# Performance work log

Hardware: AMD Instinct MI355X
Metric: run time of the kernel (lower is better)

Reference implementation:

```python
import jax, jax.numpy as jnp
import numpy as np

B, T, D = 2, 1024, 1024
H, DK = 16, 64  # n_head, d_k; inner dim = H*DK = D
INV_SQRT_DK = 1.0 / float(np.sqrt(DK))


def setup_inputs() -> dict:
    key = jax.random.key(0)
    ks = jax.random.split(key, 16)
    init = lambda k, shape: (jax.random.normal(k, shape, dtype=jnp.float32) * 0.02)
    return {
        "query": jax.random.normal(ks[0], (B, T, D), dtype=jnp.float32),
        "key": jax.random.normal(ks[1], (B, T, D), dtype=jnp.float32),
        "value": jax.random.normal(ks[2], (B, T, D), dtype=jnp.float32),
        "pos_k": jax.random.normal(ks[3], (T, T, DK), dtype=jnp.float32),
        "pos_v": jax.random.normal(ks[4], (T, T, DK), dtype=jnp.float32),
        "mask": jnp.ones((B, T, T), dtype=jnp.int32),
        "relative_attention_bias": jax.random.normal(ks[5], (1, H, T, T), dtype=jnp.float32),
        "Wq": init(ks[6], (D, D)), "bq": init(ks[7], (D,)),
        "Wk": init(ks[8], (D, D)), "bk": init(ks[9], (D,)),
        "Wv": init(ks[10], (D, D)), "bv": init(ks[11], (D,)),
        "Wo": init(ks[12], (D, D)), "bo": init(ks[13], (D,)),
    }


def reference(query, key, value, pos_k, pos_v, mask, relative_attention_bias,
              Wq, bq, Wk, bk, Wv, bv, Wo, bo):
    nb = query.shape[0]
    # projections -> (B, H, T, DK); q pre-scaled by 1/sqrt(d_k)
    q = (query @ Wq + bq).reshape(nb, -1, H, DK).transpose(0, 2, 1, 3) * INV_SQRT_DK
    k = (key @ Wk + bk).reshape(nb, -1, H, DK).transpose(0, 2, 1, 3)
    v = (value @ Wv + bv).reshape(nb, -1, H, DK).transpose(0, 2, 1, 3)

    # content scores + relative-position key scores (B, H, T, S)
    A = jnp.einsum('bhtd,bhsd->bhts', q, k)
    Bp = jnp.einsum('bhtd,tsd->bhts', q, pos_k)
    scores = A + Bp + relative_attention_bias

    # masked softmax: mask (B, T, S) -> invalid where mask == 0
    inv = (mask[:, None, :, :] == 0)  # (B, 1, T, S)
    scores = jnp.where(inv, -jnp.inf, scores)
    attn = jax.nn.softmax(scores, axis=-1)
    attn = jnp.where(inv, 0.0, attn)

    # value aggregation + relative-position value term
    x = jnp.einsum('bhts,bhsd->bhtd', attn, v)
    x = x + jnp.einsum('bhts,tsd->bhtd', attn, pos_v)

    x = x.transpose(0, 2, 1, 3).reshape(nb, -1, H * DK)  # (B, T, D)
    return x @ Wo + bo
```

## Files before the change

### kernel.cpp

```cpp
#include <hip/hip_runtime.h>


#define DEV __device__ __forceinline__

typedef short bf16x8 __attribute__((ext_vector_type(8)));
typedef short bf16x4 __attribute__((ext_vector_type(4)));
typedef float f32x4 __attribute__((ext_vector_type(4)));

DEV short f2b(float f) {
  unsigned u = __builtin_bit_cast(unsigned, f);
  u = (u + 0x7FFFu + ((u >> 16) & 1u)) >> 16;
  return (short)u;
}
DEV float b2f(short s) {
  unsigned u = ((unsigned)(unsigned short)s) << 16;
  return __builtin_bit_cast(float, u);
}

#define MFMA(a, b, c) __builtin_amdgcn_mfma_f32_16x16x32_bf16(a, b, c, 0, 0, 0)

DEV void gload16(const void* g, void* l) {
  __builtin_amdgcn_global_load_lds(
      (const __attribute__((address_space(1))) void*)g,
      (__attribute__((address_space(3))) void*)l, 16, 0, 0);
}

__global__ __launch_bounds__(256) void k_cvt3(
    const float* __restrict__ a, const float* __restrict__ b, const float* __restrict__ c,
    short* __restrict__ oa, short* __restrict__ ob, short* __restrict__ oc) {
  const float* src = blockIdx.y == 0 ? a : (blockIdx.y == 1 ? b : c);
  short* dst = blockIdx.y == 0 ? oa : (blockIdx.y == 1 ? ob : oc);
  size_t i = ((size_t)blockIdx.x * 256 + threadIdx.x) * 8;
  float4 p0 = *(const float4*)(src + i);
  float4 p1 = *(const float4*)(src + i + 4);
  bf16x8 o;
  o[0] = f2b(p0.x); o[1] = f2b(p0.y); o[2] = f2b(p0.z); o[3] = f2b(p0.w);
  o[4] = f2b(p1.x); o[5] = f2b(p1.y); o[6] = f2b(p1.z); o[7] = f2b(p1.w);
  *(bf16x8*)(dst + i) = o;
}

__global__ __launch_bounds__(256) void k_wtrans4(
    const float* __restrict__ w0, const float* __restrict__ w1,
    const float* __restrict__ w2, const float* __restrict__ w3,
    short* __restrict__ o0, short* __restrict__ o1,
    short* __restrict__ o2, short* __restrict__ o3) {
  const float* src; short* dst;
  switch (blockIdx.z) {
    case 0: src = w0; dst = o0; break;
    case 1: src = w1; dst = o1; break;
    case 2: src = w2; dst = o2; break;
    default: src = w3; dst = o3;
  }
  __shared__ short LW[64][74];
  const int tid = threadIdx.x;
  const int k0 = blockIdx.y * 64, n0 = blockIdx.x * 64;
  {
    int c4 = (tid & 15) * 4;
#pragma unroll
    for (int i = 0; i < 4; ++i) {
      int r = (tid >> 4) + i * 16;
      float4 v = *(const float4*)(src + (size_t)(k0 + r) * 1024 + n0 + c4);
      LW[r][c4 + 0] = f2b(v.x); LW[r][c4 + 1] = f2b(v.y);
      LW[r][c4 + 2] = f2b(v.z); LW[r][c4 + 3] = f2b(v.w);
    }
  }
  __syncthreads();
  {
    int n = tid >> 2, kb = (tid & 3) * 16;
#pragma unroll
    for (int j2 = 0; j2 < 2; ++j2) {
      int kk = kb + j2 * 8;
      bf16x8 o;
#pragma unroll
      for (int j = 0; j < 8; ++j) o[j] = LW[kk + j][n];
      *(bf16x8*)(dst + (size_t)(n0 + n) * 1024 + k0 + kk) = o;
    }
  }
}

__global__ __launch_bounds__(256) void k_qkv(
    const short* __restrict__ Ain, const short* __restrict__ WT,
    const float* __restrict__ bq, const float* __restrict__ bk,
    const float* __restrict__ bv,
    short* __restrict__ qo, short* __restrict__ ko, short* __restrict__ vTo) {
  __shared__ short As[128 * 32];
  __shared__ short Bs[64 * 32];
  __shared__ short LW[128][72];
  const int tid = threadIdx.x;
  const int w = tid >> 6, l = tid & 63, lg = l >> 4, lr = l & 15;
  const int wm = w >> 1, wn = w & 1;
  const int flat = blockIdx.x + gridDim.x * blockIdx.y;
  const int flat2 = (flat & 7) * 96 + (flat >> 3);
  const int n0 = (flat2 & 15) * 64;
  const int m0 = (flat2 >> 4) * 128;
  const int seg = m0 >> 11;
  const int mseg = m0 & 2047;
  const short* Abase = Ain + ((size_t)m0 << 10);
  const short* Bbase = WT + ((size_t)seg << 20) + ((size_t)n0 << 10);
  const int srow = l >> 2, scol8 = (l & 3) * 8;
  f32x4 acc[4][2] = {};
  for (int k0 = 0; k0 < 1024; k0 += 32) {
    gload16(Abase + (size_t)((w * 2) * 16 + srow) * 1024 + k0 + scol8, &As[(w * 2) * 512]);
    gload16(Abase + (size_t)((w * 2 + 1) * 16 + srow) * 1024 + k0 + scol8, &As[(w * 2 + 1) * 512]);
    gload16(Bbase + (size_t)(w * 16 + srow) * 1024 + k0 + scol8, &Bs[w * 512]);
    __syncthreads();
    bf16x8 af[4], bf[2];
#pragma unroll
    for (int i = 0; i < 4; ++i) af[i] = *(const bf16x8*)&As[(wm * 64 + i * 16 + lr) * 32 + lg * 8];
#pragma unroll
    for (int i = 0; i < 2; ++i) bf[i] = *(const bf16x8*)&Bs[(wn * 32 + i * 16 + lr) * 32 + lg * 8];
#pragma unroll
    for (int mi = 0; mi < 4; ++mi)
#pragma unroll
      for (int ni = 0; ni < 2; ++ni) acc[mi][ni] = MFMA(af[mi], bf[ni], acc[mi][ni]);
    __syncthreads();
  }
  const float* bias = seg == 0 ? bq : (seg == 1 ? bk : bv);
  const float scale = seg == 0 ? 0.125f : 1.0f;
  float bvals[2];
#pragma unroll
  for (int ni = 0; ni < 2; ++ni) bvals[ni] = bias[n0 + wn * 32 + ni * 16 + lr];
#pragma unroll
  for (int mi = 0; mi < 4; ++mi)
#pragma unroll
    for (int ni = 0; ni < 2; ++ni)
#pragma unroll
      for (int r = 0; r < 4; ++r)
        LW[wm * 64 + mi * 16 + lg * 4 + r][wn * 32 + ni * 16 + lr] =
            f2b((acc[mi][ni][r] + bvals[ni]) * scale);
  __syncthreads();
  if (seg < 2) {
    short* dst = seg == 0 ? qo : ko;
    int r = tid >> 1, half = tid & 1;
    int m = mseg + r, b = m >> 10, t = m & 1023;
    int h = n0 >> 6;
#pragma unroll
    for (int g = 0; g < 4; ++g) {
      int dk = half * 32 + g * 8;
      bf16x8 o = *(const bf16x8*)&LW[r][dk];
      *(bf16x8*)(dst + (((size_t)(b * 16 + h) * 1024 + t) << 6) + dk) = o;
    }
  } else {
    int dkc = tid & 63, th = tid >> 6;
    int h = n0 >> 6, dk = dkc;
    int b = mseg >> 10;
    int tbase = (mseg & 1023) + th * 32;
#pragma unroll
    for (int g = 0; g < 4; ++g) {
      bf16x8 o;
#pragma unroll
      for (int e = 0; e < 8; ++e) o[e] = LW[th * 32 + g * 8 + e][dkc];
      *(bf16x8*)(vTo + (((size_t)(b * 16 + h) * 64 + dk) << 10) + tbase + g * 8) = o;
    }
  }
}

__global__ __launch_bounds__(512, 2) void k_qk(
    const short* __restrict__ q, const short* __restrict__ kmat,
    short* __restrict__ S) {
  const int bh = blockIdx.y;
  const int tid = threadIdx.x;
  const int w = tid >> 6, l = tid & 63, lg = l >> 4, lr = l & 15;
  const int wm = w >> 2, wn = w & 3;
  const int t0 = blockIdx.x * 32 + wm * 16;
  const int scol = wn * 256;
  __shared__ short LS[8][16][266];

  bf16x8 af[2];
#pragma unroll
  for (int kk = 0; kk < 2; ++kk)
    af[kk] = *(const bf16x8*)(q + ((size_t)bh * 1024 + (t0 + lr)) * 64 + kk * 32 + lg * 8);

#pragma unroll
  for (int ni = 0; ni < 16; ++ni) {
    int s = scol + ni * 16 + lr;
    const short* kp = kmat + ((size_t)bh * 1024 + s) * 64 + lg * 8;
    f32x4 a = {};
    a = MFMA(af[0], *(const bf16x8*)kp, a);
    a = MFMA(af[1], *(const bf16x8*)(kp + 32), a);
#pragma unroll
    for (int r = 0; r < 4; ++r) LS[w][lg * 4 + r][ni * 16 + lr] = f2b(a[r]);
  }
  short* sb = S + ((size_t)bh * 1024 + t0) * 1024 + scol;
  const int r2 = l >> 5, c16 = (l & 31) * 8;
#pragma unroll
  for (int rr = 0; rr < 8; ++rr) {
    int row = rr * 2 + r2;
    bf16x8 o = *(const bf16x8*)&LS[w][row][c16];
    *(bf16x8*)(sb + (size_t)row * 1024 + c16) = o;
  }
}

__global__ __launch_bounds__(256) void k_posk_exp(
    const short* __restrict__ q, const float* __restrict__ pos_k,
    const float* __restrict__ rab, const int* __restrict__ mask,
    short* __restrict__ S) {
  const int t = blockIdx.y;
  const int tid = threadIdx.x;
  const int w = tid >> 6, l = tid & 63, lg = l >> 4, lr = l & 15;
  const int sB = blockIdx.x * 256;
  const int s0 = sB + w * 64;
  __shared__ float RB[16][260];
  __shared__ int MK[2][260];
  __shared__ short SW[4][32][66];
  {
    int hr = tid >> 4, c0 = (tid & 15) * 4;
#pragma unroll
    for (int it = 0; it < 4; ++it) {
      int c = c0 + it * 64;
      float4 v = *(const float4*)(rab + ((size_t)hr * 1024 + t) * 1024 + sB + c);
      RB[hr][c] = v.x; RB[hr][c + 1] = v.y; RB[hr][c + 2] = v.z; RB[hr][c + 3] = v.w;
    }
  }
  if (tid < 128) {
    int br = tid >> 6, c = (tid & 63) * 4;
    int4 mv = *(const int4*)(mask + ((size_t)br * 1024 + t) * 1024 + sB + c);
    MK[br][c] = mv.x; MK[br][c + 1] = mv.y; MK[br][c + 2] = mv.z; MK[br][c + 3] = mv.w;
  }
  {
#pragma unroll
    for (int rr = 0; rr < 4; ++rr) {
      int row = (l >> 3) + rr * 8;
      int s8 = (l & 7) * 8;
      *(bf16x8*)&SW[w][row][s8] =
          *(const bf16x8*)(S + ((size_t)row * 1024 + t) * 1024 + s0 + s8);
    }
  }
  bf16x8 af[2][2];
#pragma unroll
  for (int mi = 0; mi < 2; ++mi)
#pragma unroll
    for (int kk = 0; kk < 2; ++kk) {
      int bh = mi * 16 + lr;
      af[mi][kk] = *(const bf16x8*)(q + ((size_t)bh * 1024 + t) * 64 + kk * 32 + lg * 8);
    }
  f32x4 acc[2][4] = {};
#pragma unroll
  for (int ni = 0; ni < 4; ++ni) {
    int s = s0 + ni * 16 + lr;
#pragma unroll
    for (int kk = 0; kk < 2; ++kk) {
      const float* pk = pos_k + ((size_t)t * 1024 + s) * 64 + kk * 32 + lg * 8;
      const float4 p0 = *(const float4*)pk;
      const float4 p1 = *(const float4*)(pk + 4);
      bf16x8 bfr;
      bfr[0] = f2b(p0.x); bfr[1] = f2b(p0.y); bfr[2] = f2b(p0.z); bfr[3] = f2b(p0.w);
      bfr[4] = f2b(p1.x); bfr[5] = f2b(p1.y); bfr[6] = f2b(p1.z); bfr[7] = f2b(p1.w);
#pragma unroll
      for (int mi = 0; mi < 2; ++mi) acc[mi][ni] = MFMA(af[mi][kk], bfr, acc[mi][ni]);
    }
  }
  __syncthreads();
#pragma unroll
  for (int ni = 0; ni < 4; ++ni) {
    int colw = w * 64 + ni * 16 + lr;
    int col = ni * 16 + lr;
    int msk0 = MK[0][colw];
    int msk1 = MK[1][colw];
#pragma unroll
    for (int r = 0; r < 4; ++r) {
      int h = lg * 4 + r;
      float bv = RB[h][colw];
      float v0 = acc[0][ni][r] + bv + b2f(SW[w][h][col]);
      float v1 = acc[1][ni][r] + bv + b2f(SW[w][16 + h][col]);
      float e0 = (msk0 == 0) ? 0.f : __expf(v0 - 10.f);
      float e1 = (msk1 == 0) ? 0.f : __expf(v1 - 10.f);
      SW[w][h][col] = f2b(e0);
      SW[w][16 + h][col] = f2b(e1);
    }
  }
#pragma unroll
  for (int rr = 0; rr < 4; ++rr) {
    int row = (l >> 3) + rr * 8;
    int s8 = (l & 7) * 8;
    bf16x8 o = *(const bf16x8*)&SW[w][row][s8];
    *(bf16x8*)(S + ((size_t)row * 1024 + t) * 1024 + s0 + s8) = o;
  }
}

__global__ __launch_bounds__(256) void k_posv(
    const short* __restrict__ S, const float* __restrict__ pos_v,
    short* __restrict__ X0p) {
  const int half = blockIdx.x;
  const int t = blockIdx.y;
  const int tid = threadIdx.x;
  const int w = tid >> 6, l = tid & 63, lg = l >> 4, lr = l & 15;
  const int mi = w >> 1;
  const int nb = (w & 1) * 2;
  __shared__ short pvT[64][132];
  f32x4 acc[2] = {};
  const int spair = tid >> 4;
  const int dk4 = (tid & 15) * 4;
  const int sbase = half * 512;
  for (int c = 0; c < 4; ++c) {
    const int sc = sbase + c * 128;
    if (c) __syncthreads();
#pragma unroll
    for (int it = 0; it < 4; ++it) {
      int srel = spair * 2 + it * 32;
      const float* p0 = pos_v + ((size_t)t * 1024 + sc + srel) * 64 + dk4;
      float4 a = *(const float4*)p0;
      float4 b = *(const float4*)(p0 + 64);
      unsigned u0 = (unsigned)(unsigned short)f2b(a.x) | ((unsigned)(unsigned short)f2b(b.x) << 16);
      unsigned u1 = (unsigned)(unsigned short)f2b(a.y) | ((unsigned)(unsigned short)f2b(b.y) << 16);
      unsigned u2 = (unsigned)(unsigned short)f2b(a.z) | ((unsigned)(unsigned short)f2b(b.z) << 16);
      unsigned u3 = (unsigned)(unsigned short)f2b(a.w) | ((unsigned)(unsigned short)f2b(b.w) << 16);
      *(unsigned*)&pvT[dk4 + 0][srel] = u0;
      *(unsigned*)&pvT[dk4 + 1][srel] = u1;
      *(unsigned*)&pvT[dk4 + 2][srel] = u2;
      *(unsigned*)&pvT[dk4 + 3][srel] = u3;
    }
    __syncthreads();
    const int bh = mi * 16 + lr;
    const short* sBp = S + ((size_t)bh * 1024 + t) * 1024 + sc;
#pragma unroll
    for (int kk = 0; kk < 4; ++kk) {
      bf16x8 afr = *(const bf16x8*)(sBp + kk * 32 + lg * 8);
#pragma unroll
      for (int ni = 0; ni < 2; ++ni) {
        int dk = (nb + ni) * 16 + lr;
        const short* pp = &pvT[dk][kk * 32 + lg * 8];
        bf16x4 lo = *(const bf16x4*)pp;
        bf16x4 hi = *(const bf16x4*)(pp + 4);
        bf16x8 bfr;
        bfr[0] = lo[0]; bfr[1] = lo[1]; bfr[2] = lo[2]; bfr[3] = lo[3];
        bfr[4] = hi[0]; bfr[5] = hi[1]; bfr[6] = hi[2]; bfr[7] = hi[3];
        acc[ni] = MFMA(afr, bfr, acc[ni]);
      }
    }
  }
#pragma unroll
  for (int ni = 0; ni < 2; ++ni)
#pragma unroll
    for (int r = 0; r < 4; ++r) {
      int bh2 = mi * 16 + lg * 4 + r;
      int b = bh2 >> 4, h = bh2 & 15;
      int dk = (nb + ni) * 16 + lr;
      X0p[((size_t)half << 21) + ((size_t)(b * 1024 + t)) * 1024 + h * 64 + dk] =
          f2b(acc[ni][r]);
    }
}

__global__ __launch_bounds__(256) void k_av(
    const short* __restrict__ S, const short* __restrict__ vT,
    const short* __restrict__ X0p, short* __restrict__ X) {
  const int bh = blockIdx.y;
  const int tt0 = blockIdx.x * 32;
  const int tid = threadIdx.x;
  const int w = tid >> 6, l = tid & 63, lg = l >> 4, lr = l & 15;
  const int wm = w >> 1, wn = w & 1;
  const short* vbase = vT + ((size_t)bh << 16) + ((size_t)(wn * 32) << 10);
  const short* sbase = S + ((size_t)bh << 20) + ((size_t)(tt0 + wm * 16) << 10);
  f32x4 acc[2] = {};
  float lsum = 0.f;
#pragma unroll 8
  for (int kk = 0; kk < 32; ++kk) {
    bf16x8 afr = *(const bf16x8*)(sbase + ((size_t)lr << 10) + kk * 32 + lg * 8);
#pragma unroll
    for (int j = 0; j < 8; ++j) lsum += b2f(afr[j]);
#pragma unroll
    for (int ni = 0; ni < 2; ++ni) {
      bf16x8 bfr = *(const bf16x8*)(vbase + ((size_t)(ni * 16 + lr) << 10) + kk * 32 + lg * 8);
      acc[ni] = MFMA(afr, bfr, acc[ni]);
    }
  }
  lsum += __shfl_xor(lsum, 16);
  lsum += __shfl_xor(lsum, 32);
  const int b = bh >> 4, h = bh & 15;
#pragma unroll
  for (int ni = 0; ni < 2; ++ni)
#pragma unroll
    for (int r = 0; r < 4; ++r) {
      float lrow = __shfl(lsum, lg * 4 + r);
      float inv = 1.0f / lrow;
      int tt = tt0 + wm * 16 + lg * 4 + r;
      int d = h * 64 + wn * 32 + ni * 16 + lr;
      size_t idx = ((size_t)(b * 1024 + tt)) * 1024 + d;
      X[idx] = f2b((b2f(X0p[idx]) + b2f(X0p[idx + (1u << 21)]) + acc[ni][r]) * inv);
    }
}

__global__ __launch_bounds__(256) void k_oproj(
    const short* __restrict__ X, const short* __restrict__ WT,
    const float* __restrict__ bias, float* __restrict__ out) {
  __shared__ short As[64 * 32];
  __shared__ short Bs[64 * 32];
  const int tid = threadIdx.x;
  const int w = tid >> 6, l = tid & 63, lg = l >> 4, lr = l & 15;
  const int wm = w >> 1, wn = w & 1;
  const int n0 = blockIdx.x * 64;
  const int m0 = blockIdx.y * 64;
  const short* Abase = X + ((size_t)m0 << 10);
  const short* Bbase = WT + ((size_t)n0 << 10);
  const int srow = l >> 2, scol8 = (l & 3) * 8;
  f32x4 acc[2][2] = {};
  for (int k0 = 0; k0 < 1024; k0 += 32) {
    gload16(Abase + (size_t)(w * 16 + srow) * 1024 + k0 + scol8, &As[w * 512]);
    gload16(Bbase + (size_t)(w * 16 + srow) * 1024 + k0 + scol8, &Bs[w * 512]);
    __syncthreads();
    bf16x8 af[2], bf[2];
#pragma unroll
    for (int i = 0; i < 2; ++i) af[i] = *(const bf16x8*)&As[(wm * 32 + i * 16 + lr) * 32 + lg * 8];
#pragma unroll
    for (int i = 0; i < 2; ++i) bf[i] = *(const bf16x8*)&Bs[(wn * 32 + i * 16 + lr) * 32 + lg * 8];
#pragma unroll
    for (int mi = 0; mi < 2; ++mi)
#pragma unroll
      for (int ni = 0; ni < 2; ++ni) acc[mi][ni] = MFMA(af[mi], bf[ni], acc[mi][ni]);
    __syncthreads();
  }
  float bvals[2];
#pragma unroll
  for (int ni = 0; ni < 2; ++ni) bvals[ni] = bias[n0 + wn * 32 + ni * 16 + lr];
#pragma unroll
  for (int mi = 0; mi < 2; ++mi)
#pragma unroll
    for (int ni = 0; ni < 2; ++ni)
#pragma unroll
      for (int r = 0; r < 4; ++r) {
        int m = m0 + wm * 32 + mi * 16 + lg * 4 + r;
        int n = n0 + wn * 32 + ni * 16 + lr;
        out[(size_t)m * 1024 + n] = acc[mi][ni][r] + bvals[ni];
      }
}

extern "C" void kernel_launch(void* const* d_in, const int* in_sizes, int n_in,
                              void* d_out, int out_size, void* d_ws, size_t ws_size,
                              hipStream_t stream) {
  (void)in_sizes; (void)n_in; (void)out_size; (void)ws_size;
  const float* query = (const float*)d_in[0];
  const float* key   = (const float*)d_in[1];
  const float* value = (const float*)d_in[2];
  const float* pos_k = (const float*)d_in[3];
  const float* pos_v = (const float*)d_in[4];
  const int*   mask  = (const int*)d_in[5];
  const float* rab   = (const float*)d_in[6];
  const float* Wq = (const float*)d_in[7];
  const float* bq = (const float*)d_in[8];
  const float* Wk = (const float*)d_in[9];
  const float* bk = (const float*)d_in[10];
  const float* Wv = (const float*)d_in[11];
  const float* bv = (const float*)d_in[12];
  const float* Wo = (const float*)d_in[13];
  const float* bo = (const float*)d_in[14];
  float* out = (float*)d_out;

  const size_t M2 = 2ull * 1024 * 1024;
  short* q   = (short*)d_ws;
  short* k   = q + M2;
  short* vT  = k + M2;
  short* S   = vT + M2;
  short* X0p = S + 32ull * 1024 * 1024;
  short* X   = X0p + 2 * M2;
  short* qin = X + M2;
  short* kin = qin + M2;
  short* vin = kin + M2;
  short* WqT = vin + M2;
  short* WkT = WqT + 1024 * 1024;
  short* WvT = WkT + 1024 * 1024;
  short* WoT = WvT + 1024 * 1024;

  k_cvt3<<<dim3(1024, 3), dim3(256), 0, stream>>>(query, key, value, qin, kin, vin);
  k_wtrans4<<<dim3(16, 16, 4), dim3(256), 0, stream>>>(Wq, Wk, Wv, Wo, WqT, WkT, WvT, WoT);
  k_qkv<<<dim3(16, 48), dim3(256), 0, stream>>>(qin, WqT, bq, bk, bv, q, k, vT);
  k_qk<<<dim3(32, 32), dim3(512), 0, stream>>>(q, k, S);
  k_posk_exp<<<dim3(4, 1024), dim3(256), 0, stream>>>(q, pos_k, rab, mask, S);
  k_posv<<<dim3(2, 1024), dim3(256), 0, stream>>>(S, pos_v, X0p);
  k_av<<<dim3(32, 32), dim3(256), 0, stream>>>(S, vT, X0p, X);
  k_oproj<<<dim3(16, 32), dim3(256), 0, stream>>>(X, WoT, bo, out);
}
```

Baseline: 311.7 us.

## Fuse pos_v aggregation into pos_k/exp kernel with fp32 atomic accumulation

```diff
diff --git a/kernel.cpp b/kernel.cpp
--- a/kernel.cpp
+++ b/kernel.cpp
@@ -191,40 +191,65 @@
   }
 }
 
-__global__ __launch_bounds__(256) void k_posk_exp(
+__global__ __launch_bounds__(256) void k_posk_pv(
     const short* __restrict__ q, const float* __restrict__ pos_k,
-    const float* __restrict__ rab, const int* __restrict__ mask,
-    short* __restrict__ S) {
+    const float* __restrict__ pos_v, const float* __restrict__ rab,
+    const int* __restrict__ mask, short* __restrict__ S,
+    float* __restrict__ X0f) {
   const int t = blockIdx.y;
   const int tid = threadIdx.x;
   const int w = tid >> 6, l = tid & 63, lg = l >> 4, lr = l & 15;
-  const int sB = blockIdx.x * 256;
-  const int s0 = sB + w * 64;
-  __shared__ float RB[16][260];
-  __shared__ int MK[2][260];
-  __shared__ short SW[4][32][66];
+  const int sB = blockIdx.x * 128;
+  const int s0 = sB + w * 32;
+  __shared__ float RB[16][132];
+  __shared__ int MK[2][132];
+  __shared__ short SW[4][32][36];
+  __shared__ short pvT[4][64][36];
+
+  float4 PK[2][2][2];
+#pragma unroll
+  for (int ni = 0; ni < 2; ++ni) {
+    int s = s0 + ni * 16 + lr;
+#pragma unroll
+    for (int kk = 0; kk < 2; ++kk) {
+      const float* pk = pos_k + ((size_t)t * 1024 + s) * 64 + kk * 32 + lg * 8;
+      PK[ni][kk][0] = *(const float4*)pk;
+      PK[ni][kk][1] = *(const float4*)(pk + 4);
+    }
+  }
+  float4 rv[2];
   {
     int hr = tid >> 4, c0 = (tid & 15) * 4;
 #pragma unroll
-    for (int it = 0; it < 4; ++it) {
+    for (int it = 0; it < 2; ++it)
+      rv[it] = *(const float4*)(rab + ((size_t)hr * 1024 + t) * 1024 + sB + c0 + it * 64);
+  }
+  int4 mv = {1, 1, 1, 1};
+  if (tid < 64) {
+    int br = tid >> 5, c = (tid & 31) * 4;
+    mv = *(const int4*)(mask + ((size_t)br * 1024 + t) * 1024 + sB + c);
+  }
+  {
+    int row = l & 31, ch = l >> 5;
+#pragma unroll
+    for (int rr = 0; rr < 2; ++rr) {
+      int c8 = ch * 8 + rr * 16;
+      *(bf16x8*)&SW[w][row][c8] =
+          *(const bf16x8*)(S + ((size_t)row * 1024 + t) * 1024 + s0 + c8);
+    }
+  }
+  {
+    int hr = tid >> 4, c0 = (tid & 15) * 4;
+#pragma unroll
+    for (int it = 0; it < 2; ++it) {
       int c = c0 + it * 64;
-      float4 v = *(const float4*)(rab + ((size_t)hr * 1024 + t) * 1024 + sB + c);
-      RB[hr][c] = v.x; RB[hr][c + 1] = v.y; RB[hr][c + 2] = v.z; RB[hr][c + 3] = v.w;
-    }
-  }
-  if (tid < 128) {
-    int br = tid >> 6, c = (tid & 63) * 4;
-    int4 mv = *(const int4*)(mask + ((size_t)br * 1024 + t) * 1024 + sB + c);
+      RB[hr][c] = rv[it].x; RB[hr][c + 1] = rv[it].y;
+      RB[hr][c + 2] = rv[it].z; RB[hr][c + 3] = rv[it].w;
+    }
+  }
+  if (tid < 64) {
+    int br = tid >> 5, c = (tid & 31) * 4;
     MK[br][c] = mv.x; MK[br][c + 1] = mv.y; MK[br][c + 2] = mv.z; MK[br][c + 3] = mv.w;
-  }
-  {
-#pragma unroll
-    for (int rr = 0; rr < 4; ++rr) {
-      int row = (l >> 3) + rr * 8;
-      int s8 = (l & 7) * 8;
-      *(bf16x8*)&SW[w][row][s8] =
-          *(const bf16x8*)(S + ((size_t)row * 1024 + t) * 1024 + s0 + s8);
-    }
   }
   bf16x8 af[2][2];
 #pragma unroll
@@ -234,27 +259,42 @@
       int bh = mi * 16 + lr;
       af[mi][kk] = *(const bf16x8*)(q + ((size_t)bh * 1024 + t) * 64 + kk * 32 + lg * 8);
     }
-  f32x4 acc[2][4] = {};
-#pragma unroll
-  for (int ni = 0; ni < 4; ++ni) {
-    int s = s0 + ni * 16 + lr;
+  f32x4 acc[2][2] = {};
+#pragma unroll
+  for (int ni = 0; ni < 2; ++ni)
 #pragma unroll
     for (int kk = 0; kk < 2; ++kk) {
-      const float* pk = pos_k + ((size_t)t * 1024 + s) * 64 + kk * 32 + lg * 8;
-      const float4 p0 = *(const float4*)pk;
-      const float4 p1 = *(const float4*)(pk + 4);
       bf16x8 bfr;
-      bfr[0] = f2b(p0.x); bfr[1] = f2b(p0.y); bfr[2] = f2b(p0.z); bfr[3] = f2b(p0.w);
-      bfr[4] = f2b(p1.x); bfr[5] = f2b(p1.y); bfr[6] = f2b(p1.z); bfr[7] = f2b(p1.w);
+      bfr[0] = f2b(PK[ni][kk][0].x); bfr[1] = f2b(PK[ni][kk][0].y);
+      bfr[2] = f2b(PK[ni][kk][0].z); bfr[3] = f2b(PK[ni][kk][0].w);
+      bfr[4] = f2b(PK[ni][kk][1].x); bfr[5] = f2b(PK[ni][kk][1].y);
+      bfr[6] = f2b(PK[ni][kk][1].z); bfr[7] = f2b(PK[ni][kk][1].w);
 #pragma unroll
       for (int mi = 0; mi < 2; ++mi) acc[mi][ni] = MFMA(af[mi][kk], bfr, acc[mi][ni]);
     }
+  {
+    int sp = l & 15;
+#pragma unroll
+    for (int c = 0; c < 4; ++c) {
+      int dk4 = (l >> 4) * 4 + c * 16;
+      const float* p0 = pos_v + ((size_t)t * 1024 + s0 + sp * 2) * 64 + dk4;
+      float4 a = *(const float4*)p0;
+      float4 b = *(const float4*)(p0 + 64);
+      unsigned u0 = (unsigned)(unsigned short)f2b(a.x) | ((unsigned)(unsigned short)f2b(b.x) << 16);
+      unsigned u1 = (unsigned)(unsigned short)f2b(a.y) | ((unsigned)(unsigned short)f2b(b.y) << 16);
+      unsigned u2 = (unsigned)(unsigned short)f2b(a.z) | ((unsigned)(unsigned short)f2b(b.z) << 16);
+      unsigned u3 = (unsigned)(unsigned short)f2b(a.w) | ((unsigned)(unsigned short)f2b(b.w) << 16);
+      *(unsigned*)&pvT[w][dk4 + 0][sp * 2] = u0;
+      *(unsigned*)&pvT[w][dk4 + 1][sp * 2] = u1;
+      *(unsigned*)&pvT[w][dk4 + 2][sp * 2] = u2;
+      *(unsigned*)&pvT[w][dk4 + 3][sp * 2] = u3;
+    }
   }
   __syncthreads();
 #pragma unroll
-  for (int ni = 0; ni < 4; ++ni) {
-    int colw = w * 64 + ni * 16 + lr;
+  for (int ni = 0; ni < 2; ++ni) {
     int col = ni * 16 + lr;
+    int colw = w * 32 + col;
     int msk0 = MK[0][colw];
     int msk1 = MK[1][colw];
 #pragma unroll
@@ -269,81 +309,54 @@
       SW[w][16 + h][col] = f2b(e1);
     }
   }
-#pragma unroll
-  for (int rr = 0; rr < 4; ++rr) {
-    int row = (l >> 3) + rr * 8;
-    int s8 = (l & 7) * 8;
-    bf16x8 o = *(const bf16x8*)&SW[w][row][s8];
-    *(bf16x8*)(S + ((size_t)row * 1024 + t) * 1024 + s0 + s8) = o;
-  }
-}
-
-__global__ __launch_bounds__(256) void k_posv(
-    const short* __restrict__ S, const float* __restrict__ pos_v,
-    short* __restrict__ X0p) {
-  const int half = blockIdx.x;
-  const int t = blockIdx.y;
-  const int tid = threadIdx.x;
-  const int w = tid >> 6, l = tid & 63, lg = l >> 4, lr = l & 15;
-  const int mi = w >> 1;
-  const int nb = (w & 1) * 2;
-  __shared__ short pvT[64][132];
-  f32x4 acc[2] = {};
-  const int spair = tid >> 4;
-  const int dk4 = (tid & 15) * 4;
-  const int sbase = half * 512;
-  for (int c = 0; c < 4; ++c) {
-    const int sc = sbase + c * 128;
-    if (c) __syncthreads();
-#pragma unroll
-    for (int it = 0; it < 4; ++it) {
-      int srel = spair * 2 + it * 32;
-      const float* p0 = pos_v + ((size_t)t * 1024 + sc + srel) * 64 + dk4;
-      float4 a = *(const float4*)p0;
-      float4 b = *(const float4*)(p0 + 64);
-      unsigned u0 = (unsigned)(unsigned short)f2b(a.x) | ((unsigned)(unsigned short)f2b(b.x) << 16);
-      unsigned u1 = (unsigned)(unsigned short)f2b(a.y) | ((unsigned)(unsigned short)f2b(b.y) << 16);
-      unsigned u2 = (unsigned)(unsigned short)f2b(a.z) | ((unsigned)(unsigned short)f2b(b.z) << 16);
-      unsigned u3 = (unsigned)(unsigned short)f2b(a.w) | ((unsigned)(unsigned short)f2b(b.w) << 16);
-      *(unsigned*)&pvT[dk4 + 0][srel] = u0;
-      *(unsigned*)&pvT[dk4 + 1][srel] = u1;
-      *(unsigned*)&pvT[dk4 + 2][srel] = u2;
-      *(unsigned*)&pvT[dk4 + 3][srel] = u3;
-    }
-    __syncthreads();
-    const int bh = mi * 16 + lr;
-    const short* sBp = S + ((size_t)bh * 1024 + t) * 1024 + sc;
-#pragma unroll
-    for (int kk = 0; kk < 4; ++kk) {
-      bf16x8 afr = *(const bf16x8*)(sBp + kk * 32 + lg * 8);
-#pragma unroll
-      for (int ni = 0; ni < 2; ++ni) {
-        int dk = (nb + ni) * 16 + lr;
-        const short* pp = &pvT[dk][kk * 32 + lg * 8];
-        bf16x4 lo = *(const bf16x4*)pp;
-        bf16x4 hi = *(const bf16x4*)(pp + 4);
-        bf16x8 bfr;
-        bfr[0] = lo[0]; bfr[1] = lo[1]; bfr[2] = lo[2]; bfr[3] = lo[3];
-        bfr[4] = hi[0]; bfr[5] = hi[1]; bfr[6] = hi[2]; bfr[7] = hi[3];
-        acc[ni] = MFMA(afr, bfr, acc[ni]);
+  f32x4 apv[2][4] = {};
+  {
+    bf16x8 afr[2];
+#pragma unroll
+    for (int mi = 0; mi < 2; ++mi) {
+      const short* sp = &SW[w][mi * 16 + lr][lg * 8];
+      bf16x4 lo = *(const bf16x4*)sp;
+      bf16x4 hi = *(const bf16x4*)(sp + 4);
+      afr[mi][0] = lo[0]; afr[mi][1] = lo[1]; afr[mi][2] = lo[2]; afr[mi][3] = lo[3];
+      afr[mi][4] = hi[0]; afr[mi][5] = hi[1]; afr[mi][6] = hi[2]; afr[mi][7] = hi[3];
+    }
+#pragma unroll
+    for (int ni = 0; ni < 4; ++ni) {
+      const short* pp = &pvT[w][ni * 16 + lr][lg * 8];
+      bf16x4 lo = *(const bf16x4*)pp;
+      bf16x4 hi = *(const bf16x4*)(pp + 4);
+      bf16x8 bfr;
+      bfr[0] = lo[0]; bfr[1] = lo[1]; bfr[2] = lo[2]; bfr[3] = lo[3];
+      bfr[4] = hi[0]; bfr[5] = hi[1]; bfr[6] = hi[2]; bfr[7] = hi[3];
+#pragma unroll
+      for (int mi = 0; mi < 2; ++mi) apv[mi][ni] = MFMA(afr[mi], bfr, apv[mi][ni]);
+    }
+  }
+  {
+    int row = l & 31, ch = l >> 5;
+#pragma unroll
+    for (int rr = 0; rr < 2; ++rr) {
+      int c8 = ch * 8 + rr * 16;
+      bf16x8 o = *(const bf16x8*)&SW[w][row][c8];
+      *(bf16x8*)(S + ((size_t)row * 1024 + t) * 1024 + s0 + c8) = o;
+    }
+  }
+#pragma unroll
+  for (int mi = 0; mi < 2; ++mi)
+#pragma unroll
+    for (int ni = 0; ni < 4; ++ni)
+#pragma unroll
+      for (int r = 0; r < 4; ++r) {
+        int bh2 = mi * 16 + lg * 4 + r;
+        int b = bh2 >> 4, h = bh2 & 15;
+        int dk = ni * 16 + lr;
+        atomicAdd(&X0f[((size_t)(b * 1024 + t)) * 1024 + h * 64 + dk], apv[mi][ni][r]);
       }
-    }
-  }
-#pragma unroll
-  for (int ni = 0; ni < 2; ++ni)
-#pragma unroll
-    for (int r = 0; r < 4; ++r) {
-      int bh2 = mi * 16 + lg * 4 + r;
-      int b = bh2 >> 4, h = bh2 & 15;
-      int dk = (nb + ni) * 16 + lr;
-      X0p[((size_t)half << 21) + ((size_t)(b * 1024 + t)) * 1024 + h * 64 + dk] =
-          f2b(acc[ni][r]);
-    }
 }
 
 __global__ __launch_bounds__(256) void k_av(
     const short* __restrict__ S, const short* __restrict__ vT,
-    const short* __restrict__ X0p, short* __restrict__ X) {
+    const float* __restrict__ X0f, short* __restrict__ X) {
   const int bh = blockIdx.y;
   const int tt0 = blockIdx.x * 32;
   const int tid = threadIdx.x;
@@ -376,7 +389,7 @@
       int tt = tt0 + wm * 16 + lg * 4 + r;
       int d = h * 64 + wn * 32 + ni * 16 + lr;
       size_t idx = ((size_t)(b * 1024 + tt)) * 1024 + d;
-      X[idx] = f2b((b2f(X0p[idx]) + b2f(X0p[idx + (1u << 21)]) + acc[ni][r]) * inv);
+      X[idx] = f2b((X0f[idx] + acc[ni][r]) * inv);
     }
 }
 
@@ -450,8 +463,8 @@
   short* k   = q + M2;
   short* vT  = k + M2;
   short* S   = vT + M2;
-  short* X0p = S + 32ull * 1024 * 1024;
-  short* X   = X0p + 2 * M2;
+  float* X0f = (float*)(S + 32ull * 1024 * 1024);
+  short* X   = (short*)(X0f + M2);
   short* qin = X + M2;
   short* kin = qin + M2;
   short* vin = kin + M2;
@@ -460,12 +473,12 @@
   short* WvT = WkT + 1024 * 1024;
   short* WoT = WvT + 1024 * 1024;
 
+  hipMemsetAsync(X0f, 0, M2 * sizeof(float), stream);
   k_cvt3<<<dim3(1024, 3), dim3(256), 0, stream>>>(query, key, value, qin, kin, vin);
   k_wtrans4<<<dim3(16, 16, 4), dim3(256), 0, stream>>>(Wq, Wk, Wv, Wo, WqT, WkT, WvT, WoT);
   k_qkv<<<dim3(16, 48), dim3(256), 0, stream>>>(qin, WqT, bq, bk, bv, q, k, vT);
   k_qk<<<dim3(32, 32), dim3(512), 0, stream>>>(q, k, S);
-  k_posk_exp<<<dim3(4, 1024), dim3(256), 0, stream>>>(q, pos_k, rab, mask, S);
-  k_posv<<<dim3(2, 1024), dim3(256), 0, stream>>>(S, pos_v, X0p);
-  k_av<<<dim3(32, 32), dim3(256), 0, stream>>>(S, vT, X0p, X);
+  k_posk_pv<<<dim3(8, 1024), dim3(256), 0, stream>>>(q, pos_k, pos_v, rab, mask, S, X0f);
+  k_av<<<dim3(32, 32), dim3(256), 0, stream>>>(S, vT, X0f, X);
   k_oproj<<<dim3(16, 32), dim3(256), 0, stream>>>(X, WoT, bo, out);
 }
```

Measured after the change: 373.2 us. 19.7% more time.
